# Performance work log

Hardware: AMD Instinct MI355X
Metric: run time of the kernel (lower is better)

## Reference

```python
import jax, jax.numpy as jnp
import numpy as np

H = 16            # num_attention_heads
START_RATIO = 0.1
RECENT_RATIO = 0.4
THETA = 10000.0
CHUNK = 256       # hard-coded chunk_size in source
CLIP = 1e4        # nan_to_num posinf/neginf bound


def _rope_cos_sin(T, D, dtype):
    inv_freq = 1.0 / (THETA ** (jnp.arange(0, D, 2, dtype=jnp.float32) / D))
    freqs = jnp.arange(T, dtype=jnp.float32)[:, None] * inv_freq[None, :]  # [T, D/2]
    emb = jnp.concatenate([freqs, freqs], axis=-1)                          # [T, D]
    return jnp.cos(emb).astype(dtype), jnp.sin(emb).astype(dtype)


def _apply_rope(x, cos, sin):
    # x: [B,H,T,D]; cos/sin: [T,D] broadcast over B,H
    d = x.shape[-1] // 2
    rot = jnp.concatenate([-x[..., d:], x[..., :d]], axis=-1)
    return x * cos + rot * sin


def setup_inputs() -> dict:
    key = jax.random.key(0)
    k0, k1, k2, k3, k4 = jax.random.split(key, 5)
    B, T, Dm = 1, 2048, 2048
    scale = 1.0 / np.sqrt(Dm).astype(np.float32)
    return {
        "hidden_states": jax.random.normal(k0, (B, T, Dm), jnp.float32),
        "Wq": jax.random.normal(k1, (Dm, Dm), jnp.float32) * scale,
        "Wk": jax.random.normal(k2, (Dm, Dm), jnp.float32) * scale,
        "Wv": jax.random.normal(k3, (Dm, Dm), jnp.float32) * scale,
        "Wo": jax.random.normal(k4, (Dm, Dm), jnp.float32) * scale,
    }


def reference(hidden_states, Wq, Wk, Wv, Wo):
    B, T, Dm = hidden_states.shape
    D = Dm // H
    hs = jnp.nan_to_num(hidden_states, nan=0.0, posinf=CLIP, neginf=-CLIP)

    def proj(W):  # torch Linear: x @ W.T, then [B,T,H,D] -> [B,H,T,D]
        return (hs @ W.T).reshape(B, T, H, D).transpose(0, 2, 1, 3)

    q, k, v = proj(Wq), proj(Wk), proj(Wv)
    cos, sin = _rope_cos_sin(T, D, hs.dtype)
    q = _apply_rope(q, cos, sin)
    k = _apply_rope(k, cos, sin)

    # start+recent keep mask (past_key_value=None -> k_len == T)
    k_len = T
    sb = max(0, min(int(START_RATIO * k_len), k_len))
    rb = max(0, min(int(RECENT_RATIO * k_len), k_len - sb))
    pos = jnp.arange(k_len)
    keep = (pos < sb) | (pos >= k_len - rb)          # [K]

    MIN = jnp.finfo(hs.dtype).min
    scores = jnp.einsum('bhqd,bhkd->bhqk', q, k) / jnp.sqrt(jnp.asarray(D, hs.dtype))
    scores = jnp.where(keep, scores, MIN)
    probs = jax.nn.softmax(scores, axis=-1)          # [B,H,T,K]

    # CaM merge of evicted V into recent window, driven by the LAST query row.
    evict = k_len - rb                               # static python int
    last = probs[..., -1, :]                         # [B,H,K]
    mean_attn = last[..., evict + 1:].mean(axis=-1) + 1e-6
    p = jnp.clip(last[..., evict] / mean_attn, 0.0, 1.0)
    p = jnp.nan_to_num(p, nan=0.0, posinf=1.0, neginf=0.0)
    u = jax.random.uniform(jax.random.key(42), p.shape, p.dtype)
    bern = (u < p).astype(v.dtype)                   # [B,H]
    v_e = v[..., evict, :] * bern[..., None] / rb    # [B,H,D]
    v_merged = v.at[..., evict + 1:, :].add(v_e[..., None, :])

    # Chunked loop effect: only the last chunk's AV uses merged V.
    last_start = ((T - 1) // CHUNK) * CHUNK
    out_pre = jnp.einsum('bhqk,bhkd->bhqd', probs[:, :, :last_start], v)
    out_last = jnp.einsum('bhqk,bhkd->bhqd', probs[:, :, last_start:], v_merged)
    out = jnp.concatenate([out_pre, out_last], axis=2)   # [B,H,T,D]

    out = out.transpose(0, 2, 1, 3).reshape(B, T, Dm) @ Wo.T
    return jnp.nan_to_num(out, nan=0.0, posinf=CLIP, neginf=-CLIP)
```

## Files before the change

### kernel.cpp

```cpp
#include <hip/hip_runtime.h>
#include <stdint.h>

#define T_SEQ 2048
#define DM    2048
#define NH    16
#define HD    128
#define SB    204
#define EV    1229
#define RB    819
#define NRECF 818.0f
#define LAST_START 1792
#define SCALE 0.08838834764831845f

typedef __attribute__((ext_vector_type(8))) short short8;
typedef __attribute__((ext_vector_type(4))) short short4v;
typedef __attribute__((ext_vector_type(4))) float f32x4;

__device__ __forceinline__ unsigned short f2bf(float f) {
  uint32_t u = __float_as_uint(f);
  u += 0x7fffu + ((u >> 16) & 1u);
  return (unsigned short)(u >> 16);
}
__device__ __forceinline__ float bf2f(unsigned short s) {
  return __uint_as_float(((uint32_t)s) << 16);
}
__device__ __forceinline__ void gload16(const void* g, void* l) {
  __builtin_amdgcn_global_load_lds((const __attribute__((address_space(1))) void*)g,
                                   (__attribute__((address_space(3))) void*)l,
                                   16, 0, 0);
}
__device__ __forceinline__ float n2n(float v) {
  if (isnan(v)) return 0.0f;
  if (isinf(v)) return v > 0.0f ? 10000.0f : -10000.0f;
  return v;
}

__global__ __launch_bounds__(256) void cvt_kernel(
    const float* __restrict__ hs, const float* __restrict__ wq,
    const float* __restrict__ wk, const float* __restrict__ wv,
    const float* __restrict__ wo, unsigned short* __restrict__ hsb,
    unsigned short* __restrict__ wqb, unsigned short* __restrict__ wkb,
    unsigned short* __restrict__ wvb, unsigned short* __restrict__ wob) {
  int gid = blockIdx.x * 256 + threadIdx.x;
  int region = gid >> 20;
  int off4 = (gid & 1048575) * 4;
  const float* src; unsigned short* dst;
  switch (region) {
    case 0: src = hs; dst = hsb; break;
    case 1: src = wq; dst = wqb; break;
    case 2: src = wk; dst = wkb; break;
    case 3: src = wv; dst = wvb; break;
    default: src = wo; dst = wob; break;
  }
  float4 v = *(const float4*)(src + off4);
  if (region == 0) { v.x = n2n(v.x); v.y = n2n(v.y); v.z = n2n(v.z); v.w = n2n(v.w); }
  ushort4 o;
  o.x = f2bf(v.x); o.y = f2bf(v.y); o.z = f2bf(v.z); o.w = f2bf(v.w);
  *(ushort4*)(dst + off4) = o;
}

__global__ __launch_bounds__(256) void cs_kernel(float* __restrict__ cst, float* __restrict__ snt) {
  int idx = blockIdx.x * 256 + threadIdx.x;
  int t = idx >> 6, i = idx & 63;
  float inv = (float)exp(-(double)i * log(10000.0) / 64.0);
  float ang = (float)t * inv;
  cst[idx] = (float)cos((double)ang);
  snt[idx] = (float)sin((double)ang);
}

__device__ __forceinline__ void gemm_mainloop64(
    const unsigned short* __restrict__ A, const unsigned short* __restrict__ B,
    unsigned short* As, unsigned short* Bs, int m0, int n0, int k0, int ksteps,
    int tid, f32x4 (&acc)[4][4]) {
  int w = tid >> 6, lane = tid & 63;
  int wm = w >> 1, wn = w & 1;
  int q4 = lane >> 4, r = lane & 15;
  f32x4 zero = {0.f, 0.f, 0.f, 0.f};
  #pragma unroll
  for (int mi = 0; mi < 4; mi++)
    #pragma unroll
    for (int ni = 0; ni < 4; ni++) acc[mi][ni] = zero;
  int srow = w * 32 + (lane >> 3);
  int swz = ((lane & 7) ^ (lane >> 3)) * 16;
  const char* Ag = (const char*)(A + (size_t)(m0 + srow) * DM) + swz + k0 * 2;
  const char* Bg = (const char*)(B + (size_t)(n0 + srow) * DM) + swz + k0 * 2;
  unsigned short* Asl = As + w * 2048;
  unsigned short* Bsl = Bs + w * 2048;
  for (int s = 0; s < ksteps; s++) {
    __syncthreads();
    #pragma unroll
    for (int g = 0; g < 4; g++) {
      gload16(Ag + g * (8 * DM * 2), Asl + g * 512);
      gload16(Bg + g * (8 * DM * 2), Bsl + g * 512);
    }
    Ag += 128; Bg += 128;
    __syncthreads();
    #pragma unroll
    for (int kh = 0; kh < 2; kh++) {
      int pcs = ((kh * 4 + q4) ^ (r & 7)) * 8;
      short8 a[4], b[4];
      #pragma unroll
      for (int mi = 0; mi < 4; mi++)
        a[mi] = *(const short8*)(As + (wm * 64 + mi * 16 + r) * 64 + pcs);
      #pragma unroll
      for (int ni = 0; ni < 4; ni++)
        b[ni] = *(const short8*)(Bs + ((ni & 1) * 64 + wn * 32 + (ni >> 1) * 16 + r) * 64 + pcs);
      #pragma unroll
      for (int mi = 0; mi < 4; mi++)
        #pragma unroll
        for (int ni = 0; ni < 4; ni++)
          acc[mi][ni] = __builtin_amdgcn_mfma_f32_16x16x32_bf16(a[mi], b[ni], acc[mi][ni], 0, 0, 0);
    }
  }
}

__global__ __launch_bounds__(256, 3) void gemm_qkv_kernel(
    const unsigned short* __restrict__ hsb, const unsigned short* __restrict__ wqb,
    const unsigned short* __restrict__ wkb, const unsigned short* __restrict__ wvb,
    const float* __restrict__ cst, const float* __restrict__ snt,
    unsigned short* __restrict__ qbf, unsigned short* __restrict__ kbf,
    unsigned short* __restrict__ vbT) {
  __shared__ __align__(16) unsigned short LDSBUF[17408];
  unsigned short* As = LDSBUF;
  unsigned short* Bs = LDSBUF + 8192;
  int z = blockIdx.z;
  const unsigned short* B = (z == 0) ? wqb : (z == 1) ? wkb : wvb;
  int m0 = blockIdx.y * 128, n0 = blockIdx.x * 128;
  f32x4 acc[4][4];
  gemm_mainloop64(hsb, B, As, Bs, m0, n0, 0, DM / 64, threadIdx.x, acc);
  int tid = threadIdx.x, w = tid >> 6, lane = tid & 63;
  int wm = w >> 1, wn = w & 1, q4 = lane >> 4, r = lane & 15;
  int h = n0 >> 7;
  if (z < 2) {
    unsigned short* dst = (z == 0) ? qbf : kbf;
    #pragma unroll
    for (int mi = 0; mi < 4; mi++)
      #pragma unroll
      for (int p = 0; p < 2; p++) {
        int d = wn * 32 + p * 16 + r;
        #pragma unroll
        for (int g = 0; g < 4; g++) {
          int t = m0 + wm * 64 + mi * 16 + q4 * 4 + g;
          float c = cst[t * 64 + d], s = snt[t * 64 + d];
          float x0 = acc[mi][2 * p][g], x1 = acc[mi][2 * p + 1][g];
          dst[((size_t)h * T_SEQ + t) * HD + d]      = f2bf(x0 * c - x1 * s);
          dst[((size_t)h * T_SEQ + t) * HD + d + 64] = f2bf(x1 * c + x0 * s);
        }
      }
  } else {
    __syncthreads();
    #pragma unroll
    for (int mi = 0; mi < 4; mi++)
      #pragma unroll
      for (int ni = 0; ni < 4; ni++) {
        int c = (ni & 1) * 64 + wn * 32 + (ni >> 1) * 16 + r;
        int tl = wm * 64 + mi * 16 + q4 * 4;
        short4v pv;
        pv[0] = (short)f2bf(acc[mi][ni][0]);
        pv[1] = (short)f2bf(acc[mi][ni][1]);
        pv[2] = (short)f2bf(acc[mi][ni][2]);
        pv[3] = (short)f2bf(acc[mi][ni][3]);
        *(short4v*)(LDSBUF + c * 136 + tl) = pv;
      }
    __syncthreads();
    int d = tid >> 1, th = tid & 1;
    unsigned short* gdst = vbT + ((size_t)h * HD + d) * T_SEQ + m0 + th * 64;
    const unsigned short* lsrc = LDSBUF + d * 136 + th * 64;
    #pragma unroll
    for (int j = 0; j < 8; j++)
      *(short8*)(gdst + j * 8) = *(const short8*)(lsrc + j * 8);
  }
}

__device__ __forceinline__ void attn_body(
    int kb, const unsigned short* Kt, const unsigned short* Vt,
    const unsigned short* indv, unsigned short* Psw,
    const short8 (&aq)[4], f32x4 (&o)[8], f32x4& o9, float (&evf)[4],
    int q4, int r) {
  f32x4 zero = {0.f, 0.f, 0.f, 0.f};
  int rsw = (r >> 1) & 3;
  f32x4 s0 = zero, s1 = zero;
  #pragma unroll
  for (int c = 0; c < 4; c++) {
    int pc = ((c * 4 + q4) ^ r) * 8;
    short8 bk0 = *(const short8*)(Kt + r * 128 + pc);
    short8 bk1 = *(const short8*)(Kt + (16 + r) * 128 + pc);
    s0 = __builtin_amdgcn_mfma_f32_16x16x32_bf16(aq[c], bk0, s0, 0, 0, 0);
    s1 = __builtin_amdgcn_mfma_f32_16x16x32_bf16(aq[c], bk1, s1, 0, 0, 0);
  }
  int kg0 = kb + r, kg1 = kb + 16 + r;
  bool keep0 = (kg0 < SB) || (kg0 >= EV);
  bool keep1 = (kg1 < SB) || (kg1 >= EV);
  #pragma unroll
  for (int g = 0; g < 4; g++) {
    float p0 = keep0 ? __expf(fmaf(s0[g], SCALE, -8.0f)) : 0.0f;
    float p1 = keep1 ? __expf(fmaf(s1[g], SCALE, -8.0f)) : 0.0f;
    if (kb == 1216 && kg0 == EV) evf[g] = p0;
    int row = q4 * 4 + g;
    int psw = (row >> 1) & 3;
    Psw[row * 32 + (((r >> 3) ^ psw) * 8) + (r & 7)]       = f2bf(p0);
    Psw[row * 32 + ((((r >> 3) + 2) ^ psw) * 8) + (r & 7)] = f2bf(p1);
  }
  short8 pa = *(const short8*)(Psw + r * 32 + (q4 ^ rsw) * 8);
  #pragma unroll
  for (int ni = 0; ni < 8; ni++) {
    short8 bv = *(const short8*)(Vt + (ni * 16 + r) * 32 + (q4 ^ rsw) * 8);
    o[ni] = __builtin_amdgcn_mfma_f32_16x16x32_bf16(pa, bv, o[ni], 0, 0, 0);
  }
  short8 bind = *(const short8*)(indv + r * 32 + (q4 ^ rsw) * 8);
  o9 = __builtin_amdgcn_mfma_f32_16x16x32_bf16(pa, bind, o9, 0, 0, 0);
}

__global__ __launch_bounds__(256, 2) void attn_kernel(
    const unsigned short* __restrict__ qbf, const unsigned short* __restrict__ kbf,
    const unsigned short* __restrict__ vbT, unsigned short* __restrict__ atb,
    float* __restrict__ attnf_s, float* __restrict__ Ssum, float* __restrict__ lst) {
  __shared__ __align__(16) unsigned short KtS[2][2][4096];
  __shared__ __align__(16) unsigned short VtS[2][2][4096];
  __shared__ __align__(16) unsigned short Ps[4][512];
  __shared__ __align__(16) unsigned short Ind[3 * 512];
  int tid = threadIdx.x, w = tid >> 6, lane = tid & 63;
  int q4 = lane >> 4, r = lane & 15;
  int h = blockIdx.y;
  int qb = blockIdx.x * 64 + w * 16;

  for (int idx = tid; idx < 3 * 512; idx += 256) {
    int v = idx >> 9, n = (idx >> 5) & 15, j = idx & 31;
    float val = 0.f;
    if (n == 0) val = 1.f;
    else if (n == 1) val = (v == 1) ? (j >= 14 ? 1.f : 0.f) : (v == 2 ? 1.f : 0.f);
    Ind[v * 512 + n * 32 + (((j >> 3) ^ ((n >> 1) & 3)) * 8) + (j & 7)] = f2bf(val);
  }

  short8 aq[4];
  {
    const unsigned short* qrow = qbf + ((size_t)h * T_SEQ + qb + r) * HD;
    #pragma unroll
    for (int c = 0; c < 4; c++) aq[c] = *(const short8*)(qrow + c * 32 + q4 * 8);
  }
  f32x4 zero = {0.f, 0.f, 0.f, 0.f};
  f32x4 o[8], o9;
  #pragma unroll
  for (int ni = 0; ni < 8; ni++) o[ni] = zero;
  o9 = zero;
  float evf[4] = {0.f, 0.f, 0.f, 0.f};

  const char* Kbase = (const char*)(kbf + (size_t)h * T_SEQ * HD);
  int krow0 = w * 8 + q4, krow1 = krow0 + 4;
  const char* Kg0 = Kbase + krow0 * 256 + ((r ^ (krow0 & 15)) * 16);
  const char* Kg1 = Kbase + krow1 * 256 + ((r ^ (krow1 & 15)) * 16);
  const char* Vbase = (const char*)(vbT + (size_t)h * HD * T_SEQ);
  int vsrc = ((lane & 3) ^ ((lane >> 3) & 3)) * 16;
  const char* Vg0 = Vbase + (size_t)(w * 32 + (lane >> 2)) * 4096 + vsrc;
  const char* Vg1 = Vg0 + 16 * 4096;

  auto issue_chunk = [&](int ci, int db) {
    int kb = (ci < 4) ? ci * 64 : 1216 + (ci - 4) * 64;
    gload16(Kg0 + kb * 256,         &KtS[db][0][w * 1024]);
    gload16(Kg1 + kb * 256,         &KtS[db][0][w * 1024 + 512]);
    gload16(Kg0 + (kb + 32) * 256,  &KtS[db][1][w * 1024]);
    gload16(Kg1 + (kb + 32) * 256,  &KtS[db][1][w * 1024 + 512]);
    gload16(Vg0 + kb * 2,           &VtS[db][0][w * 1024]);
    gload16(Vg1 + kb * 2,           &VtS[db][0][w * 1024 + 512]);
    gload16(Vg0 + (kb + 32) * 2,    &VtS[db][1][w * 1024]);
    gload16(Vg1 + (kb + 32) * 2,    &VtS[db][1][w * 1024 + 512]);
  };

  issue_chunk(0, 0);
  for (int ci = 0; ci < 17; ci++) {
    int db = ci & 1;
    int kb = (ci < 4) ? ci * 64 : 1216 + (ci - 4) * 64;
    const unsigned short* indA = Ind + ((ci < 4) ? 0 : (ci == 4) ? 512 : 1024);
    const unsigned short* indB = Ind + ((ci < 4) ? 0 : 1024);
    __syncthreads();
    if (ci < 16) issue_chunk(ci + 1, db ^ 1);
    attn_body(kb,      KtS[db][0], VtS[db][0], indA, &Ps[w][0], aq, o, o9, evf, q4, r);
    attn_body(kb + 32, KtS[db][1], VtS[db][1], indB, &Ps[w][0], aq, o, o9, evf, q4, r);
  }

  float invl[4], srn[4], evn[4];
  #pragma unroll
  for (int g = 0; g < 4; g++) {
    float l  = __shfl(o9[g], lane & 48, 64);
    float sr = __shfl(o9[g], (lane & 48) | 1, 64);
    float ev = __shfl(evf[g], (lane & 48) | 13, 64);
    invl[g] = 1.0f / l;
    srn[g] = sr * invl[g];
    evn[g] = ev * invl[g];
  }
  if (blockIdx.x < (LAST_START / 64)) {
    #pragma unroll
    for (int ni = 0; ni < 8; ni++)
      #pragma unroll
      for (int g = 0; g < 4; g++)
        atb[(size_t)(qb + q4 * 4 + g) * DM + h * HD + ni * 16 + r] = f2bf(o[ni][g] * invl[g]);
  } else {
    #pragma unroll
    for (int ni = 0; ni < 8; ni++)
      #pragma unroll
      for (int g = 0; g < 4; g++)
        attnf_s[(size_t)(qb - LAST_START + q4 * 4 + g) * DM + h * HD + ni * 16 + r] = o[ni][g] * invl[g];
  }
  if (r == 0) {
    #pragma unroll
    for (int g = 0; g < 4; g++) {
      int t = qb + q4 * 4 + g;
      if (t >= LAST_START) Ssum[h * 256 + (t - LAST_START)] = srn[g];
      if (t == T_SEQ - 1) { lst[h * 2] = evn[g]; lst[h * 2 + 1] = srn[g]; }
    }
  }
}

__device__ __forceinline__ void tf_round(uint32_t& x0, uint32_t& x1, int rot) {
  x0 += x1;
  x1 = (x1 << rot) | (x1 >> (32 - rot));
  x1 ^= x0;
}
__device__ __forceinline__ float bern_scale(int hh, const float* lst) {
  const uint32_t k0 = 0u, k1 = 42u, k2 = 0x1BD11BDAu ^ k0 ^ k1;
  uint32_t x0 = (uint32_t)(hh & 7), x1 = (uint32_t)((hh & 7) + 8);
  x0 += k0; x1 += k1;
  tf_round(x0, x1, 13); tf_round(x0, x1, 15); tf_round(x0, x1, 26); tf_round(x0, x1, 6);
  x0 += k1; x1 += k2 + 1u;
  tf_round(x0, x1, 17); tf_round(x0, x1, 29); tf_round(x0, x1, 16); tf_round(x0, x1, 24);
  x0 += k2; x1 += k0 + 2u;
  tf_round(x0, x1, 13); tf_round(x0, x1, 15); tf_round(x0, x1, 26); tf_round(x0, x1, 6);
  x0 += k0; x1 += k1 + 3u;
  tf_round(x0, x1, 17); tf_round(x0, x1, 29); tf_round(x0, x1, 16); tf_round(x0, x1, 24);
  x0 += k1; x1 += k2 + 4u;
  tf_round(x0, x1, 13); tf_round(x0, x1, 15); tf_round(x0, x1, 26); tf_round(x0, x1, 6);
  x0 += k2; x1 += k0 + 5u;
  uint32_t bits = (hh < 8) ? x0 : x1;
  float u = __uint_as_float((bits >> 9) | 0x3f800000u) - 1.0f;
  float evp = lst[hh * 2], srp = lst[hh * 2 + 1];
  float mean = srp * (1.0f / NRECF) + 1e-6f;
  float p = evp / mean;
  p = fminf(fmaxf(p, 0.0f), 1.0f);
  if (!(p == p)) p = 0.0f;
  return (u < p) ? (1.0f / (float)RB) : 0.0f;
}

__global__ __launch_bounds__(256) void fixup_kernel(
    const float* __restrict__ attnf_s, const float* __restrict__ Ssum,
    const float* __restrict__ lst, const unsigned short* __restrict__ vbT,
    unsigned short* __restrict__ atb) {
  int idx = blockIdx.x * 256 + threadIdx.x;
  int t2 = idx >> 11, n = idx & 2047;
  int h = n >> 7, d = n & 127;
  float bsc = bern_scale(h, lst);
  float v = attnf_s[idx];
  v += Ssum[h * 256 + t2] * bsc * bf2f(vbT[((size_t)h * HD + d) * T_SEQ + EV]);
  atb[(size_t)(t2 + LAST_START) * DM + n] = f2bf(v);
}

__global__ __launch_bounds__(256, 2) void gemm_out_kernel(
    const unsigned short* __restrict__ atb, const unsigned short* __restrict__ wob,
    float* __restrict__ out) {
  __shared__ __align__(16) unsigned short LDSBUF[16384];
  unsigned short* As = LDSBUF;
  unsigned short* Bs = LDSBUF + 8192;
  int m0 = blockIdx.y * 128, n0 = blockIdx.x * 128;
  int kz = blockIdx.z;
  f32x4 acc[4][4];
  gemm_mainloop64(atb, wob, As, Bs, m0, n0, kz * 1024, 16, threadIdx.x, acc);
  int tid = threadIdx.x, w = tid >> 6, lane = tid & 63;
  int wm = w >> 1, wn = w & 1, q4 = lane >> 4, r = lane & 15;
  #pragma unroll
  for (int mi = 0; mi < 4; mi++)
    #pragma unroll
    for (int ni = 0; ni < 4; ni++) {
      int c = n0 + (ni & 1) * 64 + wn * 32 + (ni >> 1) * 16 + r;
      #pragma unroll
      for (int g = 0; g < 4; g++) {
        int t = m0 + wm * 64 + mi * 16 + q4 * 4 + g;
        atomicAdd(&out[(size_t)t * DM + c], acc[mi][ni][g]);
      }
    }
}

extern "C" void kernel_launch(void* const* d_in, const int* in_sizes, int n_in,
                              void* d_out, int out_size, void* d_ws, size_t ws_size,
                              hipStream_t stream) {
  const float* hs = (const float*)d_in[0];
  const float* Wq = (const float*)d_in[1];
  const float* Wk = (const float*)d_in[2];
  const float* Wv = (const float*)d_in[3];
  const float* Wo = (const float*)d_in[4];
  char* ws = (char*)d_ws;
  const size_t MB = 1024 * 1024;
  unsigned short* hsb = (unsigned short*)(ws + 0);
  unsigned short* wqb = (unsigned short*)(ws + 8 * MB);
  unsigned short* wkb = (unsigned short*)(ws + 16 * MB);
  unsigned short* wvb = (unsigned short*)(ws + 24 * MB);
  unsigned short* wob = (unsigned short*)(ws + 32 * MB);
  unsigned short* qbf = (unsigned short*)(ws + 40 * MB);
  unsigned short* kbf = (unsigned short*)(ws + 48 * MB);
  unsigned short* vbT = (unsigned short*)(ws + 56 * MB);
  unsigned short* atb = (unsigned short*)(ws + 64 * MB);
  float* attnf_s = (float*)(ws + 72 * MB);
  float* cst = (float*)(ws + 74 * MB);
  float* snt = (float*)(ws + 74 * MB + 524288);
  float* Ssum = (float*)(ws + 75 * MB);
  float* lst = (float*)(ws + 75 * MB + 16384);

  hipMemsetAsync(d_out, 0, (size_t)out_size * sizeof(float), stream);
  cvt_kernel<<<20480, 256, 0, stream>>>(hs, Wq, Wk, Wv, Wo, hsb, wqb, wkb, wvb, wob);
  cs_kernel<<<512, 256, 0, stream>>>(cst, snt);
  gemm_qkv_kernel<<<dim3(16, 16, 3), 256, 0, stream>>>(hsb, wqb, wkb, wvb, cst, snt, qbf, kbf, vbT);
  attn_kernel<<<dim3(32, 16), 256, 0, stream>>>(qbf, kbf, vbT, atb, attnf_s, Ssum, lst);
  fixup_kernel<<<2048, 256, 0, stream>>>(attnf_s, Ssum, lst, vbT, atb);
  gemm_out_kernel<<<dim3(16, 16, 2), 256, 0, stream>>>(atb, wob, (float*)d_out);
}
```

Measured before the change: 260.4 us.

## Double-buffer GEMM LDS loads, fold RoPE table into convert, replace atomics with partials

The GEMM main loop now double-buffers LDS, prefetching the next K-step's tiles while the current one is computed. This drops one barrier per step and hides global-to-LDS latency, but doubles LDS per block, so the QKV kernel's occupancy hint falls from 3 to 2. The cos/sin table build is merged into the convert kernel to save a launch. The output GEMM's split-K atomics and memset are replaced by two partial buffers plus an add kernel, which also applies nan_to_num. That adds a write and a reread of 32MB of partials in place of the atomic traffic.

```diff
diff --git a/kernel.cpp b/kernel.cpp
--- a/kernel.cpp
+++ b/kernel.cpp
@@ -40,7 +40,17 @@
     const float* __restrict__ wk, const float* __restrict__ wv,
     const float* __restrict__ wo, unsigned short* __restrict__ hsb,
     unsigned short* __restrict__ wqb, unsigned short* __restrict__ wkb,
-    unsigned short* __restrict__ wvb, unsigned short* __restrict__ wob) {
+    unsigned short* __restrict__ wvb, unsigned short* __restrict__ wob,
+    float* __restrict__ cst, float* __restrict__ snt) {
+  if (blockIdx.x >= 20480) {
+    int idx = (blockIdx.x - 20480) * 256 + threadIdx.x;
+    int t = idx >> 6, i = idx & 63;
+    float inv = (float)exp(-(double)i * log(10000.0) / 64.0);
+    float ang = (float)t * inv;
+    cst[idx] = (float)cos((double)ang);
+    snt[idx] = (float)sin((double)ang);
+    return;
+  }
   int gid = blockIdx.x * 256 + threadIdx.x;
   int region = gid >> 20;
   int off4 = (gid & 1048575) * 4;
@@ -59,19 +69,10 @@
   *(ushort4*)(dst + off4) = o;
 }
 
-__global__ __launch_bounds__(256) void cs_kernel(float* __restrict__ cst, float* __restrict__ snt) {
-  int idx = blockIdx.x * 256 + threadIdx.x;
-  int t = idx >> 6, i = idx & 63;
-  float inv = (float)exp(-(double)i * log(10000.0) / 64.0);
-  float ang = (float)t * inv;
-  cst[idx] = (float)cos((double)ang);
-  snt[idx] = (float)sin((double)ang);
-}
-
-__device__ __forceinline__ void gemm_mainloop64(
+__device__ __forceinline__ void gemm_mainloop64_db(
     const unsigned short* __restrict__ A, const unsigned short* __restrict__ B,
-    unsigned short* As, unsigned short* Bs, int m0, int n0, int k0, int ksteps,
-    int tid, f32x4 (&acc)[4][4]) {
+    unsigned short* LDSBUF,
+    int m0, int n0, int k0, int ksteps, int tid, f32x4 (&acc)[4][4]) {
   int w = tid >> 6, lane = tid & 63;
   int wm = w >> 1, wn = w & 1;
   int q4 = lane >> 4, r = lane & 15;
@@ -84,17 +85,26 @@
   int swz = ((lane & 7) ^ (lane >> 3)) * 16;
   const char* Ag = (const char*)(A + (size_t)(m0 + srow) * DM) + swz + k0 * 2;
   const char* Bg = (const char*)(B + (size_t)(n0 + srow) * DM) + swz + k0 * 2;
-  unsigned short* Asl = As + w * 2048;
-  unsigned short* Bsl = Bs + w * 2048;
+  unsigned short* AsB[2] = {LDSBUF + w * 2048, LDSBUF + 16384 + w * 2048};
+  unsigned short* BsB[2] = {LDSBUF + 8192 + w * 2048, LDSBUF + 24576 + w * 2048};
+  #pragma unroll
+  for (int g = 0; g < 4; g++) {
+    gload16(Ag + g * (8 * DM * 2), AsB[0] + g * 512);
+    gload16(Bg + g * (8 * DM * 2), BsB[0] + g * 512);
+  }
   for (int s = 0; s < ksteps; s++) {
+    int db = s & 1;
     __syncthreads();
-    #pragma unroll
-    for (int g = 0; g < 4; g++) {
-      gload16(Ag + g * (8 * DM * 2), Asl + g * 512);
-      gload16(Bg + g * (8 * DM * 2), Bsl + g * 512);
+    if (s + 1 < ksteps) {
+      #pragma unroll
+      for (int g = 0; g < 4; g++) {
+        gload16(Ag + 128 + g * (8 * DM * 2), AsB[db ^ 1] + g * 512);
+        gload16(Bg + 128 + g * (8 * DM * 2), BsB[db ^ 1] + g * 512);
+      }
     }
     Ag += 128; Bg += 128;
-    __syncthreads();
+    const unsigned short* As = LDSBUF + (db ? 16384 : 0);
+    const unsigned short* Bs = LDSBUF + (db ? 24576 : 8192);
     #pragma unroll
     for (int kh = 0; kh < 2; kh++) {
       int pcs = ((kh * 4 + q4) ^ (r & 7)) * 8;
@@ -114,20 +124,18 @@
   }
 }
 
-__global__ __launch_bounds__(256, 3) void gemm_qkv_kernel(
+__global__ __launch_bounds__(256, 2) void gemm_qkv_kernel(
     const unsigned short* __restrict__ hsb, const unsigned short* __restrict__ wqb,
     const unsigned short* __restrict__ wkb, const unsigned short* __restrict__ wvb,
     const float* __restrict__ cst, const float* __restrict__ snt,
     unsigned short* __restrict__ qbf, unsigned short* __restrict__ kbf,
     unsigned short* __restrict__ vbT) {
-  __shared__ __align__(16) unsigned short LDSBUF[17408];
-  unsigned short* As = LDSBUF;
-  unsigned short* Bs = LDSBUF + 8192;
+  __shared__ __align__(16) unsigned short LDSBUF[32768];
   int z = blockIdx.z;
   const unsigned short* B = (z == 0) ? wqb : (z == 1) ? wkb : wvb;
   int m0 = blockIdx.y * 128, n0 = blockIdx.x * 128;
   f32x4 acc[4][4];
-  gemm_mainloop64(hsb, B, As, Bs, m0, n0, 0, DM / 64, threadIdx.x, acc);
+  gemm_mainloop64_db(hsb, B, LDSBUF, m0, n0, 0, DM / 64, threadIdx.x, acc);
   int tid = threadIdx.x, w = tid >> 6, lane = tid & 63;
   int wm = w >> 1, wn = w & 1, q4 = lane >> 4, r = lane & 15;
   int h = n0 >> 7;
@@ -355,14 +363,13 @@
 
 __global__ __launch_bounds__(256, 2) void gemm_out_kernel(
     const unsigned short* __restrict__ atb, const unsigned short* __restrict__ wob,
-    float* __restrict__ out) {
-  __shared__ __align__(16) unsigned short LDSBUF[16384];
-  unsigned short* As = LDSBUF;
-  unsigned short* Bs = LDSBUF + 8192;
+    float* __restrict__ part0, float* __restrict__ part1) {
+  __shared__ __align__(16) unsigned short LDSBUF[32768];
   int m0 = blockIdx.y * 128, n0 = blockIdx.x * 128;
   int kz = blockIdx.z;
+  float* part = kz ? part1 : part0;
   f32x4 acc[4][4];
-  gemm_mainloop64(atb, wob, As, Bs, m0, n0, kz * 1024, 16, threadIdx.x, acc);
+  gemm_mainloop64_db(atb, wob, LDSBUF, m0, n0, kz * 1024, 16, threadIdx.x, acc);
   int tid = threadIdx.x, w = tid >> 6, lane = tid & 63;
   int wm = w >> 1, wn = w & 1, q4 = lane >> 4, r = lane & 15;
   #pragma unroll
@@ -373,9 +380,20 @@
       #pragma unroll
       for (int g = 0; g < 4; g++) {
         int t = m0 + wm * 64 + mi * 16 + q4 * 4 + g;
-        atomicAdd(&out[(size_t)t * DM + c], acc[mi][ni][g]);
+        part[(size_t)t * DM + c] = acc[mi][ni][g];
       }
     }
+}
+
+__global__ __launch_bounds__(256) void add_kernel(
+    const float* __restrict__ p0, const float* __restrict__ p1, float* __restrict__ out) {
+  int i4 = (blockIdx.x * 256 + threadIdx.x) * 4;
+  float4 a = *(const float4*)(p0 + i4);
+  float4 b = *(const float4*)(p1 + i4);
+  float4 o;
+  o.x = n2n(a.x + b.x); o.y = n2n(a.y + b.y);
+  o.z = n2n(a.z + b.z); o.w = n2n(a.w + b.w);
+  *(float4*)(out + i4) = o;
 }
 
 extern "C" void kernel_launch(void* const* d_in, const int* in_sizes, int n_in,
@@ -398,16 +416,17 @@
   unsigned short* vbT = (unsigned short*)(ws + 56 * MB);
   unsigned short* atb = (unsigned short*)(ws + 64 * MB);
   float* attnf_s = (float*)(ws + 72 * MB);
-  float* cst = (float*)(ws + 74 * MB);
-  float* snt = (float*)(ws + 74 * MB + 524288);
-  float* Ssum = (float*)(ws + 75 * MB);
-  float* lst = (float*)(ws + 75 * MB + 16384);
-
-  hipMemsetAsync(d_out, 0, (size_t)out_size * sizeof(float), stream);
-  cvt_kernel<<<20480, 256, 0, stream>>>(hs, Wq, Wk, Wv, Wo, hsb, wqb, wkb, wvb, wob);
-  cs_kernel<<<512, 256, 0, stream>>>(cst, snt);
+  float* part0 = (float*)(ws + 74 * MB);
+  float* part1 = (float*)(ws + 90 * MB);
+  float* cst = (float*)(ws + 106 * MB);
+  float* snt = (float*)(ws + 106 * MB + 524288);
+  float* Ssum = (float*)(ws + 107 * MB);
+  float* lst = (float*)(ws + 107 * MB + 16384);
+
+  cvt_kernel<<<20992, 256, 0, stream>>>(hs, Wq, Wk, Wv, Wo, hsb, wqb, wkb, wvb, wob, cst, snt);
   gemm_qkv_kernel<<<dim3(16, 16, 3), 256, 0, stream>>>(hsb, wqb, wkb, wvb, cst, snt, qbf, kbf, vbT);
   attn_kernel<<<dim3(32, 16), 256, 0, stream>>>(qbf, kbf, vbT, atb, attnf_s, Ssum, lst);
   fixup_kernel<<<2048, 256, 0, stream>>>(attnf_s, Ssum, lst, vbT, atb);
-  gemm_out_kernel<<<dim3(16, 16, 2), 256, 0, stream>>>(atb, wob, (float*)d_out);
-}
+  gemm_out_kernel<<<dim3(16, 16, 2), 256, 0, stream>>>(atb, wob, part0, part1);
+  add_kernel<<<4096, 256, 0, stream>>>(part0, part1, (float*)d_out);
+}
```

After: 248.2 us. -4.7%, faster.
